# Performance work log

Hardware: AMD Instinct MI355X
Metric: run time of the kernel (lower is better)

## Reference

```python
import jax, jax.numpy as jnp
import numpy as np
import math

B, L, E, H = 512, 200, 64, 4
D = E // H
NEG = jnp.float32(-(2.0 ** 32) + 1.0)


def setup_inputs() -> dict:
    key = jax.random.key(0)
    ks = jax.random.split(key, 12)
    inp = jax.random.normal(ks[0], (B, L, E), dtype=jnp.float32)
    # realistic variable-length histories: mask[b, t] = t < len_b, len_b in [1, L]
    lens = jax.random.randint(ks[1], (B, 1), 1, L + 1)
    mask = jnp.arange(L)[None, :] < lens  # [B, L] bool
    s = 1.0 / math.sqrt(E)
    pos_enc = jax.random.normal(ks[2], (1, L, E), dtype=jnp.float32)
    Wk = jax.random.uniform(ks[3], (E, E), jnp.float32, -s, s)
    bk = jnp.zeros((E,), jnp.float32)
    Wv = jax.random.uniform(ks[4], (E, E), jnp.float32, -s, s)
    bv = jnp.zeros((E,), jnp.float32)
    Wq = jax.random.uniform(ks[5], (E, E), jnp.float32, -s, s)
    bq = jnp.zeros((E,), jnp.float32)
    Wf = jax.random.uniform(ks[6], (E, E), jnp.float32, -s, s)
    bf = jnp.zeros((E,), jnp.float32)
    return {"input": inp, "mask": mask, "pos_enc": pos_enc,
            "Wk": Wk, "bk": bk, "Wv": Wv, "bv": bv,
            "Wq": Wq, "bq": bq, "Wf": Wf, "bf": bf}


def reference(input, mask, pos_enc, Wk, bk, Wv, bv, Wq, bq, Wf, bf):
    x = input + pos_enc  # [B, L, E]
    # project and split heads: [B, H, L, D]
    def split(t):
        return t.reshape(B, L, H, D).transpose(0, 2, 1, 3)
    k = split(x @ Wk.T + bk)
    v = split(x @ Wv.T + bv)
    q = split(x @ Wq.T + bq) / math.sqrt(D)
    scores = jnp.einsum('bhqd,bhkd->bhqk', q, k)  # [B, H, L, L]
    # key_mask in torch code broadcasts over dim 3 (mask on the QUERY axis),
    # query_mask is its transpose (mask on the KEY axis). Combined: both must be valid.
    both = mask[:, None, :, None] & mask[:, None, None, :]  # [B, 1, L, L]
    scores = jnp.where(both, scores, NEG)
    attn = jax.nn.softmax(scores, axis=-1)
    # dropout is identity at inference; omitted deterministically
    out = jnp.einsum('bhqk,bhkd->bhqd', attn, v)
    out = out.transpose(0, 2, 1, 3).reshape(B, L, E)
    out = out @ Wf.T + bf
    fm = mask.astype(jnp.float32)[:, :, None]  # [B, L, 1]
    lens = jnp.sum(fm, axis=1)  # [B, 1]
    pooled = jnp.sum(out * fm, axis=1) / (lens + 1e-8)  # [B, E]
    return pooled
```

## Files before the change

### kernel.cpp

```cpp
#include <hip/hip_runtime.h>
#include <hip/hip_fp16.h>
#include <math.h>

#define Bn 512
#define Ln 200
#define En 64
#define Hn 4
#define Dn 16
#define NT13 13
#define RMAX 208
#define XS 72
#define KS 36
#define VS 212

typedef _Float16 __f16;
typedef __f16 f16x4 __attribute__((ext_vector_type(4)));
typedef __f16 f16x8 __attribute__((ext_vector_type(8)));
typedef float f32x4 __attribute__((ext_vector_type(4)));

__device__ __forceinline__ f16x8 pack8(float4 a, float4 b) {
    f16x8 r;
    r[0] = (__f16)a.x; r[1] = (__f16)a.y; r[2] = (__f16)a.z; r[3] = (__f16)a.w;
    r[4] = (__f16)b.x; r[5] = (__f16)b.y; r[6] = (__f16)b.z; r[7] = (__f16)b.w;
    return r;
}

__global__ __launch_bounds__(256, 3) void fused_kernel(
    const float* __restrict__ input, const int* __restrict__ mask,
    const float* __restrict__ pos_enc,
    const float* __restrict__ Wk, const float* __restrict__ bk,
    const float* __restrict__ Wv, const float* __restrict__ bv,
    const float* __restrict__ Wq, const float* __restrict__ bq,
    float* __restrict__ pooled)
{
    __shared__ __align__(16) __f16 xw[4][16 * XS];
    __shared__ __align__(16) __f16 Kh[RMAX * KS];
    __shared__ __align__(16) __f16 Qh[RMAX * KS];
    __shared__ __align__(16) __f16 Vt[32 * VS];
    __shared__ float red[4][16];
    __shared__ int cnt_red[4];

    const int tid  = threadIdx.x;
    const int b    = blockIdx.x >> 1, hp = blockIdx.x & 1;
    const int wave = tid >> 6, lane = tid & 63;
    const int quad = lane >> 4, ln16 = lane & 15;

    const int mv = (tid < Ln) ? mask[b * Ln + tid] : 0;

    f16x8 bfr[3][2][2];
    #pragma unroll
    for (int m = 0; m < 3; ++m) {
        const float* W = (m == 0) ? Wk : (m == 1) ? Wv : Wq;
        #pragma unroll
        for (int ct = 0; ct < 2; ++ct)
            #pragma unroll
            for (int ks = 0; ks < 2; ++ks) {
                const float4* wp = (const float4*)(W + (size_t)(hp * 32 + ct * 16 + ln16) * 64) + (ks * 8 + quad * 2);
                bfr[m][ct][ks] = pack8(wp[0], wp[1]);
            }
    }
    float bkv[2], bvv[2], bqv[2];
    #pragma unroll
    for (int ct = 0; ct < 2; ++ct) {
        int cg = hp * 32 + ct * 16 + ln16;
        bkv[ct] = bk[cg]; bvv[ct] = bv[cg]; bqv[ct] = bq[cg];
    }

    const float4* in4 = (const float4*)(input + (size_t)b * Ln * En);
    const float4* pe4 = (const float4*)pos_enc;
    __f16* myx = xw[wave];

    for (int rt = wave; rt < NT13; rt += 4) {
        #pragma unroll
        for (int i = 0; i < 4; ++i) {
            const int gi = lane + (i << 6);
            const int r = gi >> 4, c4 = gi & 15;
            const int R = rt * 16 + r;
            float4 xv = {0,0,0,0}, pv = {0,0,0,0};
            if (R < Ln) { xv = in4[R * 16 + c4]; pv = pe4[R * 16 + c4]; }
            f16x4 hx;
            hx[0] = (__f16)(xv.x + pv.x); hx[1] = (__f16)(xv.y + pv.y);
            hx[2] = (__f16)(xv.z + pv.z); hx[3] = (__f16)(xv.w + pv.w);
            *(f16x4*)(myx + r * XS + c4 * 4) = hx;
        }

        f16x8 af[2];
        #pragma unroll
        for (int ks = 0; ks < 2; ++ks)
            af[ks] = *(const f16x8*)(myx + ln16 * XS + ks * 32 + quad * 8);

        f32x4 acc[3][2];
        #pragma unroll
        for (int m = 0; m < 3; ++m)
            #pragma unroll
            for (int ct = 0; ct < 2; ++ct)
                acc[m][ct] = (f32x4){0.f, 0.f, 0.f, 0.f};
        #pragma unroll
        for (int ks = 0; ks < 2; ++ks)
            #pragma unroll
            for (int m = 0; m < 3; ++m)
                #pragma unroll
                for (int ct = 0; ct < 2; ++ct)
                    acc[m][ct] = __builtin_amdgcn_mfma_f32_16x16x32_f16(af[ks], bfr[m][ct][ks], acc[m][ct], 0, 0, 0);

        #pragma unroll
        for (int ct = 0; ct < 2; ++ct) {
            #pragma unroll
            for (int j = 0; j < 4; ++j) {
                int t = rt * 16 + quad * 4 + j;
                Kh[t * KS + ct * 16 + ln16] = (__f16)(acc[0][ct][j] + bkv[ct]);
                Qh[t * KS + ct * 16 + ln16] = (__f16)((acc[2][ct][j] + bqv[ct]) * 0.25f);
            }
            f16x4 vp;
            #pragma unroll
            for (int j = 0; j < 4; ++j) vp[j] = (__f16)(acc[1][ct][j] + bvv[ct]);
            *(f16x4*)(Vt + (ct * 16 + ln16) * VS + rt * 16 + quad * 4) = vp;
        }
    }

    int c = (mv != 0) ? 1 : 0;
    #pragma unroll
    for (int off = 32; off; off >>= 1) c += __shfl_down(c, off, 64);
    if (lane == 0) cnt_red[wave] = c;
    __syncthreads();
    const int len = cnt_red[0] + cnt_red[1] + cnt_red[2] + cnt_red[3];
    const int nt  = (len + 15) >> 4;

    const int hl   = wave >> 1;
    const int hoff = hl * 16;
    const int npair = (nt + 1) >> 1;
    f32x4 pool = {0.f, 0.f, 0.f, 0.f};

    for (int p = (wave & 1); p < npair; p += 2) {
        const int qt0 = 2 * p, qt1 = 2 * p + 1;
        const int qr1 = min(qt1 * 16 + ln16, RMAX - 1);
        const f16x4 qf0 = *(const f16x4*)(Qh + (qt0 * 16 + ln16) * KS + hoff + quad * 4);
        const f16x4 qf1 = *(const f16x4*)(Qh + qr1 * KS + hoff + quad * 4);
        f32x4 o20 = {0,0,0,0}, o21 = {0,0,0,0};
        float l0 = 0.f, l1 = 0.f;

        for (int kt = 0; kt < nt - 1; ++kt) {
            const f16x4 kf = *(const f16x4*)(Kh + (kt * 16 + ln16) * KS + hoff + quad * 4);
            const f16x4 vf = *(const f16x4*)(Vt + (hoff + ln16) * VS + kt * 16 + quad * 4);
            f32x4 s0 = __builtin_amdgcn_mfma_f32_16x16x16f16(kf, qf0, (f32x4){0,0,0,0}, 0, 0, 0);
            f32x4 s1 = __builtin_amdgcn_mfma_f32_16x16x16f16(kf, qf1, (f32x4){0,0,0,0}, 0, 0, 0);
            f16x4 pf0, pf1;
            #pragma unroll
            for (int j = 0; j < 4; ++j) {
                float p0 = __expf(fminf(s0[j], 10.f));
                float p1 = __expf(fminf(s1[j], 10.f));
                l0 += p0; l1 += p1;
                pf0[j] = (__f16)p0; pf1[j] = (__f16)p1;
            }
            o20 = __builtin_amdgcn_mfma_f32_16x16x16f16(vf, pf0, o20, 0, 0, 0);
            o21 = __builtin_amdgcn_mfma_f32_16x16x16f16(vf, pf1, o21, 0, 0, 0);
        }
        {
            const int kt = nt - 1;
            const int kbase = kt * 16 + quad * 4;
            const f16x4 kf = *(const f16x4*)(Kh + (kt * 16 + ln16) * KS + hoff + quad * 4);
            const f16x4 vf = *(const f16x4*)(Vt + (hoff + ln16) * VS + kt * 16 + quad * 4);
            f32x4 s0 = __builtin_amdgcn_mfma_f32_16x16x16f16(kf, qf0, (f32x4){0,0,0,0}, 0, 0, 0);
            f32x4 s1 = __builtin_amdgcn_mfma_f32_16x16x16f16(kf, qf1, (f32x4){0,0,0,0}, 0, 0, 0);
            f16x4 pf0, pf1;
            #pragma unroll
            for (int j = 0; j < 4; ++j) {
                const bool kok = (kbase + j) < len;
                float p0 = kok ? __expf(fminf(s0[j], 10.f)) : 0.f;
                float p1 = kok ? __expf(fminf(s1[j], 10.f)) : 0.f;
                l0 += p0; l1 += p1;
                pf0[j] = (__f16)p0; pf1[j] = (__f16)p1;
            }
            o20 = __builtin_amdgcn_mfma_f32_16x16x16f16(vf, pf0, o20, 0, 0, 0);
            o21 = __builtin_amdgcn_mfma_f32_16x16x16f16(vf, pf1, o21, 0, 0, 0);
        }

        l0 += __shfl_xor(l0, 16, 64); l0 += __shfl_xor(l0, 32, 64);
        l1 += __shfl_xor(l1, 16, 64); l1 += __shfl_xor(l1, 32, 64);
        const float rs0 = (qt0 * 16 + ln16 < len) ? 1.f / l0 : 0.f;
        const float rs1 = (qt1 * 16 + ln16 < len) ? 1.f / l1 : 0.f;
        #pragma unroll
        for (int j = 0; j < 4; ++j)
            pool[j] = fmaf(o20[j], rs0, fmaf(o21[j], rs1, pool[j]));
    }

    #pragma unroll
    for (int j = 0; j < 4; ++j) {
        #pragma unroll
        for (int off = 1; off < 16; off <<= 1) pool[j] += __shfl_xor(pool[j], off, 64);
    }
    if (ln16 == 0) {
        #pragma unroll
        for (int j = 0; j < 4; ++j) red[wave][quad * 4 + j] = pool[j];
    }
    __syncthreads();
    if (tid < 32) {
        int hl2 = tid >> 4, vd = tid & 15;
        float sres = red[hl2 * 2][vd] + red[hl2 * 2 + 1][vd];
        pooled[b * En + hp * 32 + hl2 * 16 + vd] = sres / ((float)len + 1e-8f);
    }
}

__global__ __launch_bounds__(256) void final_kernel(
    const float* __restrict__ pooled, const float* __restrict__ Wf,
    const float* __restrict__ bf_, float* __restrict__ out)
{
    __shared__ float Wfs[En * 65];
    __shared__ float accs[4][En];
    const int tid = threadIdx.x, wave = tid >> 6, lane = tid & 63;
    const int b = blockIdx.x * 4 + wave;

    const float4* Wf4 = (const float4*)Wf;
    for (int idx4 = tid; idx4 < En * 16; idx4 += 256) {
        int e = idx4 >> 4, i4 = idx4 & 15;
        float4 w = Wf4[idx4];
        Wfs[e * 65 + i4 * 4 + 0] = w.x;
        Wfs[e * 65 + i4 * 4 + 1] = w.y;
        Wfs[e * 65 + i4 * 4 + 2] = w.z;
        Wfs[e * 65 + i4 * 4 + 3] = w.w;
    }
    accs[wave][lane] = pooled[b * En + lane];
    __syncthreads();

    float s = 0.f;
    #pragma unroll
    for (int i = 0; i < En; ++i)
        s = fmaf(accs[wave][i], Wfs[lane * 65 + i], s);
    out[b * En + lane] = s + bf_[lane];
}

extern "C" void kernel_launch(void* const* d_in, const int* in_sizes, int n_in,
                              void* d_out, int out_size, void* d_ws, size_t ws_size,
                              hipStream_t stream) {
    const float* input   = (const float*)d_in[0];
    const int*   mask    = (const int*)  d_in[1];
    const float* pos_enc = (const float*)d_in[2];
    const float* Wk      = (const float*)d_in[3];
    const float* bk      = (const float*)d_in[4];
    const float* Wv      = (const float*)d_in[5];
    const float* bv      = (const float*)d_in[6];
    const float* Wq      = (const float*)d_in[7];
    const float* bq      = (const float*)d_in[8];
    const float* Wf      = (const float*)d_in[9];
    const float* bf      = (const float*)d_in[10];

    float* pooled = (float*)d_ws;
    float* out    = (float*)d_out;

    fused_kernel<<<Bn * 2, 256, 0, stream>>>(input, mask, pos_enc,
                                             Wk, bk, Wv, bv, Wq, bq, pooled);
    final_kernel<<<Bn / 4, 256, 0, stream>>>(pooled, Wf, bf, out);
}
```

Baseline: 126.6 us.

## Use 512-thread blocks, load projection A-fragments directly to registers, prefetch K/V

Doubles the block to eight waves, so each wave projects at most two 16-row tiles and the attention query-pair loop is split four ways per head instead of two. The input+pos_enc tile is loaded straight from global memory into MFMA A-fragment registers, which removes the per-wave LDS staging buffer and its write/read round trip. Both row tiles' global loads are issued before the first tile's MFMAs so their latency overlaps the weight loads and the first tile's compute. The attention loop also software-prefetches the next K/V fragments from LDS. The cost is higher register pressure under the new launch bounds and more waves idle when sequences are short.

```diff
diff --git a/kernel.cpp b/kernel.cpp
--- a/kernel.cpp
+++ b/kernel.cpp
@@ -9,7 +9,6 @@
 #define Dn 16
 #define NT13 13
 #define RMAX 208
-#define XS 72
 #define KS 36
 #define VS 212
 
@@ -18,6 +17,14 @@
 typedef __f16 f16x8 __attribute__((ext_vector_type(8)));
 typedef float f32x4 __attribute__((ext_vector_type(4)));
 
+__device__ __forceinline__ f16x8 pack8s(float4 a, float4 b, float4 pa, float4 pb) {
+    f16x8 r;
+    r[0] = (__f16)(a.x + pa.x); r[1] = (__f16)(a.y + pa.y);
+    r[2] = (__f16)(a.z + pa.z); r[3] = (__f16)(a.w + pa.w);
+    r[4] = (__f16)(b.x + pb.x); r[5] = (__f16)(b.y + pb.y);
+    r[6] = (__f16)(b.z + pb.z); r[7] = (__f16)(b.w + pb.w);
+    return r;
+}
 __device__ __forceinline__ f16x8 pack8(float4 a, float4 b) {
     f16x8 r;
     r[0] = (__f16)a.x; r[1] = (__f16)a.y; r[2] = (__f16)a.z; r[3] = (__f16)a.w;
@@ -25,7 +32,7 @@
     return r;
 }
 
-__global__ __launch_bounds__(256, 3) void fused_kernel(
+__global__ __launch_bounds__(512, 4) void fused_kernel(
     const float* __restrict__ input, const int* __restrict__ mask,
     const float* __restrict__ pos_enc,
     const float* __restrict__ Wk, const float* __restrict__ bk,
@@ -33,12 +40,11 @@
     const float* __restrict__ Wq, const float* __restrict__ bq,
     float* __restrict__ pooled)
 {
-    __shared__ __align__(16) __f16 xw[4][16 * XS];
     __shared__ __align__(16) __f16 Kh[RMAX * KS];
     __shared__ __align__(16) __f16 Qh[RMAX * KS];
     __shared__ __align__(16) __f16 Vt[32 * VS];
-    __shared__ float red[4][16];
-    __shared__ int cnt_red[4];
+    __shared__ float red[8][16];
+    __shared__ int cnt_red[8];
 
     const int tid  = threadIdx.x;
     const int b    = blockIdx.x >> 1, hp = blockIdx.x & 1;
@@ -47,6 +53,16 @@
 
     const int mv = (tid < Ln) ? mask[b * Ln + tid] : 0;
 
+    const float4* in4 = (const float4*)(input + (size_t)b * Ln * En);
+    const float4* pe4 = (const float4*)pos_enc;
+    const int rt0 = wave, rt1 = wave + 8;
+    const int R0 = rt0 * 16 + ln16, R1 = rt1 * 16 + ln16;
+    const int c4 = quad * 2;
+    float4 x00 = in4[R0 * 16 + c4],     x01 = in4[R0 * 16 + c4 + 1];
+    float4 x02 = in4[R0 * 16 + 8 + c4], x03 = in4[R0 * 16 + 8 + c4 + 1];
+    float4 p00 = pe4[R0 * 16 + c4],     p01 = pe4[R0 * 16 + c4 + 1];
+    float4 p02 = pe4[R0 * 16 + 8 + c4], p03 = pe4[R0 * 16 + 8 + c4 + 1];
+
     f16x8 bfr[3][2][2];
     #pragma unroll
     for (int m = 0; m < 3; ++m) {
@@ -66,55 +82,76 @@
         bkv[ct] = bk[cg]; bvv[ct] = bv[cg]; bqv[ct] = bq[cg];
     }
 
-    const float4* in4 = (const float4*)(input + (size_t)b * Ln * En);
-    const float4* pe4 = (const float4*)pos_enc;
-    __f16* myx = xw[wave];
-
-    for (int rt = wave; rt < NT13; rt += 4) {
-        #pragma unroll
-        for (int i = 0; i < 4; ++i) {
-            const int gi = lane + (i << 6);
-            const int r = gi >> 4, c4 = gi & 15;
-            const int R = rt * 16 + r;
-            float4 xv = {0,0,0,0}, pv = {0,0,0,0};
-            if (R < Ln) { xv = in4[R * 16 + c4]; pv = pe4[R * 16 + c4]; }
-            f16x4 hx;
-            hx[0] = (__f16)(xv.x + pv.x); hx[1] = (__f16)(xv.y + pv.y);
-            hx[2] = (__f16)(xv.z + pv.z); hx[3] = (__f16)(xv.w + pv.w);
-            *(f16x4*)(myx + r * XS + c4 * 4) = hx;
-        }
-
-        f16x8 af[2];
-        #pragma unroll
-        for (int ks = 0; ks < 2; ++ks)
-            af[ks] = *(const f16x8*)(myx + ln16 * XS + ks * 32 + quad * 8);
-
+    f16x8 af0[2];
+    af0[0] = pack8s(x00, x01, p00, p01);
+    af0[1] = pack8s(x02, x03, p02, p03);
+
+    const bool t1ok = (rt1 < NT13);
+    const bool v1   = t1ok && (R1 < Ln);
+    float4 x10 = {0,0,0,0}, x11 = {0,0,0,0}, x12 = {0,0,0,0}, x13 = {0,0,0,0};
+    float4 p10 = {0,0,0,0}, p11 = {0,0,0,0}, p12 = {0,0,0,0}, p13 = {0,0,0,0};
+    if (v1) {
+        x10 = in4[R1 * 16 + c4];     x11 = in4[R1 * 16 + c4 + 1];
+        x12 = in4[R1 * 16 + 8 + c4]; x13 = in4[R1 * 16 + 8 + c4 + 1];
+        p10 = pe4[R1 * 16 + c4];     p11 = pe4[R1 * 16 + c4 + 1];
+        p12 = pe4[R1 * 16 + 8 + c4]; p13 = pe4[R1 * 16 + 8 + c4 + 1];
+    }
+
+    {
         f32x4 acc[3][2];
         #pragma unroll
         for (int m = 0; m < 3; ++m)
             #pragma unroll
-            for (int ct = 0; ct < 2; ++ct)
-                acc[m][ct] = (f32x4){0.f, 0.f, 0.f, 0.f};
+            for (int ct = 0; ct < 2; ++ct) acc[m][ct] = (f32x4){0,0,0,0};
         #pragma unroll
         for (int ks = 0; ks < 2; ++ks)
             #pragma unroll
             for (int m = 0; m < 3; ++m)
                 #pragma unroll
                 for (int ct = 0; ct < 2; ++ct)
-                    acc[m][ct] = __builtin_amdgcn_mfma_f32_16x16x32_f16(af[ks], bfr[m][ct][ks], acc[m][ct], 0, 0, 0);
-
+                    acc[m][ct] = __builtin_amdgcn_mfma_f32_16x16x32_f16(af0[ks], bfr[m][ct][ks], acc[m][ct], 0, 0, 0);
         #pragma unroll
         for (int ct = 0; ct < 2; ++ct) {
             #pragma unroll
             for (int j = 0; j < 4; ++j) {
-                int t = rt * 16 + quad * 4 + j;
+                int t = rt0 * 16 + quad * 4 + j;
                 Kh[t * KS + ct * 16 + ln16] = (__f16)(acc[0][ct][j] + bkv[ct]);
                 Qh[t * KS + ct * 16 + ln16] = (__f16)((acc[2][ct][j] + bqv[ct]) * 0.25f);
             }
             f16x4 vp;
             #pragma unroll
             for (int j = 0; j < 4; ++j) vp[j] = (__f16)(acc[1][ct][j] + bvv[ct]);
-            *(f16x4*)(Vt + (ct * 16 + ln16) * VS + rt * 16 + quad * 4) = vp;
+            *(f16x4*)(Vt + (ct * 16 + ln16) * VS + rt0 * 16 + quad * 4) = vp;
+        }
+    }
+    if (t1ok) {
+        f16x8 af1[2];
+        af1[0] = pack8s(x10, x11, p10, p11);
+        af1[1] = pack8s(x12, x13, p12, p13);
+        f32x4 acc[3][2];
+        #pragma unroll
+        for (int m = 0; m < 3; ++m)
+            #pragma unroll
+            for (int ct = 0; ct < 2; ++ct) acc[m][ct] = (f32x4){0,0,0,0};
+        #pragma unroll
+        for (int ks = 0; ks < 2; ++ks)
+            #pragma unroll
+            for (int m = 0; m < 3; ++m)
+                #pragma unroll
+                for (int ct = 0; ct < 2; ++ct)
+                    acc[m][ct] = __builtin_amdgcn_mfma_f32_16x16x32_f16(af1[ks], bfr[m][ct][ks], acc[m][ct], 0, 0, 0);
+        #pragma unroll
+        for (int ct = 0; ct < 2; ++ct) {
+            #pragma unroll
+            for (int j = 0; j < 4; ++j) {
+                int t = rt1 * 16 + quad * 4 + j;
+                Kh[t * KS + ct * 16 + ln16] = (__f16)(acc[0][ct][j] + bkv[ct]);
+                Qh[t * KS + ct * 16 + ln16] = (__f16)((acc[2][ct][j] + bqv[ct]) * 0.25f);
+            }
+            f16x4 vp;
+            #pragma unroll
+            for (int j = 0; j < 4; ++j) vp[j] = (__f16)(acc[1][ct][j] + bvv[ct]);
+            *(f16x4*)(Vt + (ct * 16 + ln16) * VS + rt1 * 16 + quad * 4) = vp;
         }
     }
 
@@ -123,15 +160,17 @@
     for (int off = 32; off; off >>= 1) c += __shfl_down(c, off, 64);
     if (lane == 0) cnt_red[wave] = c;
     __syncthreads();
-    const int len = cnt_red[0] + cnt_red[1] + cnt_red[2] + cnt_red[3];
-    const int nt  = (len + 15) >> 4;
-
-    const int hl   = wave >> 1;
+    int len = 0;
+    #pragma unroll
+    for (int w = 0; w < 8; ++w) len += cnt_red[w];
+    const int nt = (len + 15) >> 4;
+
+    const int hl = wave >> 2;
     const int hoff = hl * 16;
     const int npair = (nt + 1) >> 1;
     f32x4 pool = {0.f, 0.f, 0.f, 0.f};
 
-    for (int p = (wave & 1); p < npair; p += 2) {
+    for (int p = (wave & 3); p < npair; p += 4) {
         const int qt0 = 2 * p, qt1 = 2 * p + 1;
         const int qr1 = min(qt1 * 16 + ln16, RMAX - 1);
         const f16x4 qf0 = *(const f16x4*)(Qh + (qt0 * 16 + ln16) * KS + hoff + quad * 4);
@@ -139,37 +178,38 @@
         f32x4 o20 = {0,0,0,0}, o21 = {0,0,0,0};
         float l0 = 0.f, l1 = 0.f;
 
+        f16x4 kf = *(const f16x4*)(Kh + ln16 * KS + hoff + quad * 4);
+        f16x4 vf = *(const f16x4*)(Vt + (hoff + ln16) * VS + quad * 4);
+
         for (int kt = 0; kt < nt - 1; ++kt) {
-            const f16x4 kf = *(const f16x4*)(Kh + (kt * 16 + ln16) * KS + hoff + quad * 4);
-            const f16x4 vf = *(const f16x4*)(Vt + (hoff + ln16) * VS + kt * 16 + quad * 4);
+            const f16x4 kfn = *(const f16x4*)(Kh + ((kt + 1) * 16 + ln16) * KS + hoff + quad * 4);
+            const f16x4 vfn = *(const f16x4*)(Vt + (hoff + ln16) * VS + (kt + 1) * 16 + quad * 4);
             f32x4 s0 = __builtin_amdgcn_mfma_f32_16x16x16f16(kf, qf0, (f32x4){0,0,0,0}, 0, 0, 0);
             f32x4 s1 = __builtin_amdgcn_mfma_f32_16x16x16f16(kf, qf1, (f32x4){0,0,0,0}, 0, 0, 0);
             f16x4 pf0, pf1;
             #pragma unroll
             for (int j = 0; j < 4; ++j) {
-                float p0 = __expf(fminf(s0[j], 10.f));
-                float p1 = __expf(fminf(s1[j], 10.f));
-                l0 += p0; l1 += p1;
-                pf0[j] = (__f16)p0; pf1[j] = (__f16)p1;
+                float q0 = __expf(fminf(s0[j], 10.f));
+                float q1 = __expf(fminf(s1[j], 10.f));
+                l0 += q0; l1 += q1;
+                pf0[j] = (__f16)q0; pf1[j] = (__f16)q1;
             }
             o20 = __builtin_amdgcn_mfma_f32_16x16x16f16(vf, pf0, o20, 0, 0, 0);
             o21 = __builtin_amdgcn_mfma_f32_16x16x16f16(vf, pf1, o21, 0, 0, 0);
+            kf = kfn; vf = vfn;
         }
         {
-            const int kt = nt - 1;
-            const int kbase = kt * 16 + quad * 4;
-            const f16x4 kf = *(const f16x4*)(Kh + (kt * 16 + ln16) * KS + hoff + quad * 4);
-            const f16x4 vf = *(const f16x4*)(Vt + (hoff + ln16) * VS + kt * 16 + quad * 4);
+            const int kbase = (nt - 1) * 16 + quad * 4;
             f32x4 s0 = __builtin_amdgcn_mfma_f32_16x16x16f16(kf, qf0, (f32x4){0,0,0,0}, 0, 0, 0);
             f32x4 s1 = __builtin_amdgcn_mfma_f32_16x16x16f16(kf, qf1, (f32x4){0,0,0,0}, 0, 0, 0);
             f16x4 pf0, pf1;
             #pragma unroll
             for (int j = 0; j < 4; ++j) {
                 const bool kok = (kbase + j) < len;
-                float p0 = kok ? __expf(fminf(s0[j], 10.f)) : 0.f;
-                float p1 = kok ? __expf(fminf(s1[j], 10.f)) : 0.f;
-                l0 += p0; l1 += p1;
-                pf0[j] = (__f16)p0; pf1[j] = (__f16)p1;
+                float q0 = kok ? __expf(fminf(s0[j], 10.f)) : 0.f;
+                float q1 = kok ? __expf(fminf(s1[j], 10.f)) : 0.f;
+                l0 += q0; l1 += q1;
+                pf0[j] = (__f16)q0; pf1[j] = (__f16)q1;
             }
             o20 = __builtin_amdgcn_mfma_f32_16x16x16f16(vf, pf0, o20, 0, 0, 0);
             o21 = __builtin_amdgcn_mfma_f32_16x16x16f16(vf, pf1, o21, 0, 0, 0);
@@ -196,7 +236,8 @@
     __syncthreads();
     if (tid < 32) {
         int hl2 = tid >> 4, vd = tid & 15;
-        float sres = red[hl2 * 2][vd] + red[hl2 * 2 + 1][vd];
+        float sres = red[hl2 * 4][vd] + red[hl2 * 4 + 1][vd]
+                   + red[hl2 * 4 + 2][vd] + red[hl2 * 4 + 3][vd];
         pooled[b * En + hp * 32 + hl2 * 16 + vd] = sres / ((float)len + 1e-8f);
     }
 }
@@ -247,7 +288,7 @@
     float* pooled = (float*)d_ws;
     float* out    = (float*)d_out;
 
-    fused_kernel<<<Bn * 2, 256, 0, stream>>>(input, mask, pos_enc,
+    fused_kernel<<<Bn * 2, 512, 0, stream>>>(input, mask, pos_enc,
                                              Wk, bk, Wv, bv, Wq, bq, pooled);
     final_kernel<<<Bn / 4, 256, 0, stream>>>(pooled, Wf, bf, out);
 }
```

Result: slower. 163.7 us (+29.3%).
